# Optimization experiments

Measured on AMD Instinct MI355X. Metric: run time of the kernel, lower is better.

The kernel has to match this reference:

```python
import jax, jax.numpy as jnp
import numpy as np
import math

BS, SEQ, LQ = 64, 2048, 128
NHEADS, D_TIME, NH, DV = 4, 128, 128, 2
D_K = D_TIME // NHEADS
T10_LO, T10_HI = 0.1, 5.0
M0_LO, M0_HI = 0.1, 10.0
XFA_MAX_DEG = 25.0
REG_H = 200


def setup_inputs() -> dict:
    key = jax.random.key(0)
    ks = jax.random.split(key, 40)
    w = lambda i, shape, s=0.05: jax.random.normal(ks[i], shape, dtype=jnp.float32) * s
    return {
        "X_fa_in": jax.random.uniform(ks[0], (BS, SEQ), dtype=jnp.float32),
        "fa_vals": jax.random.uniform(ks[1], (BS, SEQ), dtype=jnp.float32),
        "fa_mask": jax.random.bernoulli(ks[2], 0.7, (BS, SEQ)),
        "fa_len": jnp.full((BS, 1), float(SEQ), dtype=jnp.float32),
        "TR_vals": jax.random.uniform(ks[3], (BS, SEQ), dtype=jnp.float32),
        "te_lin_w": w(4, (1, 1)), "te_lin_b": w(5, (1,)),
        "te_per_w": w(6, (D_TIME - 1, 1), 1.0), "te_per_b": w(7, (D_TIME - 1,)),
        "q_w": w(8, (D_TIME, D_TIME)), "q_b": w(9, (D_TIME,)),
        "k_w": w(10, (D_TIME, D_TIME)), "k_b": w(11, (D_TIME,)),
        "att_out_w": w(12, (NH, NHEADS * DV)), "att_out_b": w(13, (NH,)),
        "gru_wih": w(14, (3 * NH, NH)), "gru_whh": w(15, (3 * NH, NH)),
        "gru_bih": w(16, (3 * NH,)), "gru_bhh": w(17, (3 * NH,)),
        "score_t10_w": w(18, (1, NH)), "score_m0_w": w(19, (1, NH)),
        "regT_w1": w(20, (REG_H, NH)), "regT_b1": w(21, (REG_H,)),
        "regT_w2": w(22, (REG_H, REG_H)), "regT_b2": w(23, (REG_H,)),
        "regT_w3": w(24, (1, REG_H)), "regT_b3": w(25, (1,)),
        "regM_w1": w(26, (REG_H, NH)), "regM_b1": w(27, (REG_H,)),
        "regM_w2": w(28, (REG_H, REG_H)), "regM_b2": w(29, (REG_H,)),
        "regM_w3": w(30, (1, REG_H)), "regM_b3": w(31, (1,)),
    }


def _time_embed(t, lw, lb, pw, pb):
    # t: (..., L) -> (..., L, D_TIME); linear(1->1) concat sin(linear(1->D_TIME-1))
    t = t[..., None]
    lin = t * lw[0, 0] + lb                      # (..., L, 1)
    per = jnp.sin(t @ pw.T + pb)                 # (..., L, D_TIME-1)
    return jnp.concatenate([lin, per], axis=-1)


def _gru(x, wih, whh, bih, bhh):
    # x: (bs, T, NH) -> (bs, T, NH), torch nn.GRU semantics, h0 = 0
    x_gates = jnp.einsum('bth,gh->btg', x, wih) + bih  # (bs, T, 3*NH)

    def step(h, xt):
        gh = h @ whh.T + bhh
        ri, zi, ni = jnp.split(xt, 3, axis=-1)
        rh, zh, nh = jnp.split(gh, 3, axis=-1)
        r = jax.nn.sigmoid(ri + rh)
        z = jax.nn.sigmoid(zi + zh)
        n = jnp.tanh(ni + r * nh)
        hn = (1.0 - z) * n + z * h
        return hn, hn

    h0 = jnp.zeros((x.shape[0], whh.shape[1]), dtype=x.dtype)
    _, hs = jax.lax.scan(step, h0, x_gates.transpose(1, 0, 2))
    return hs.transpose(1, 0, 2)


def _mlp(h, w1, b1, w2, b2, w3, b3):
    h = jax.nn.gelu(h @ w1.T + b1, approximate=False)
    h = jax.nn.gelu(h @ w2.T + b2, approximate=False)
    return h @ w3.T + b3


def reference(X_fa_in, fa_vals, fa_mask, fa_len, TR_vals,
              te_lin_w, te_lin_b, te_per_w, te_per_b,
              q_w, q_b, k_w, k_b, att_out_w, att_out_b,
              gru_wih, gru_whh, gru_bih, gru_bhh,
              score_t10_w, score_m0_w,
              regT_w1, regT_b1, regT_w2, regT_b2, regT_w3, regT_b3,
              regM_w1, regM_b1, regM_w2, regM_b2, regM_w3, regM_b3):
    bs, seq = X_fa_in.shape
    # ---- time embeddings (dropout inactive / eval) ----
    key_input = fa_vals / math.radians(XFA_MAX_DEG - 1.0)
    k_emb = _time_embed(key_input, te_lin_w, te_lin_b, te_per_w, te_per_b)   # (bs, seq, D_TIME)
    q_ref = jnp.linspace(0.0, 1.0, LQ, dtype=X_fa_in.dtype)[None, :]         # (1, LQ)
    q_emb = _time_embed(q_ref, te_lin_w, te_lin_b, te_per_w, te_per_b)       # (1, LQ, D_TIME)

    # ---- multi-time attention ----
    q = (q_emb @ q_w.T + q_b).reshape(1, LQ, NHEADS, D_K).transpose(0, 2, 1, 3)[0]  # (h, LQ, d_k)
    k = (k_emb @ k_w.T + k_b).reshape(bs, seq, NHEADS, D_K).transpose(0, 2, 1, 3)    # (bs, h, seq, d_k)
    scores = jnp.einsum('hqd,bhsd->bhqs', q, k) / jnp.sqrt(jnp.asarray(D_K, X_fa_in.dtype))
    # mask is broadcast identically across the d_v replication in the original,
    # so the per-channel softmax collapses to one softmax over keys.
    scores = jnp.where(fa_mask[:, None, None, :], scores, jnp.asarray(-1e9, scores.dtype))
    p = jax.nn.softmax(scores, axis=-1)                                      # (bs, h, LQ, seq)
    v = jnp.concatenate([X_fa_in[..., None], fa_mask.astype(X_fa_in.dtype)[..., None]], axis=-1)  # (bs, seq, 2)
    attn = jnp.einsum('bhqs,bsd->bhqd', p, v)                                # (bs, h, LQ, 2)
    concat = attn.transpose(0, 2, 1, 3).reshape(bs, LQ, NHEADS * DV)
    att_out = concat @ att_out_w.T + att_out_b                               # (bs, LQ, NH)

    # ---- GRU + attention pooling ----
    out = _gru(att_out, gru_wih, gru_whh, gru_bih, gru_bhh)                  # (bs, LQ, NH)
    sT = jax.nn.softmax(out @ score_t10_w.T, axis=1)                         # (bs, LQ, 1)
    sM = jax.nn.softmax(out @ score_m0_w.T, axis=1)
    hidden_T10 = jnp.sum(out * sT, axis=1)                                   # (bs, NH)
    hidden_M0 = jnp.sum(out * sM, axis=1)

    T10 = T10_LO + jax.nn.sigmoid(_mlp(hidden_T10, regT_w1, regT_b1, regT_w2, regT_b2, regT_w3, regT_b3)) * (T10_HI - T10_LO)  # (bs, 1)
    M0 = M0_LO + jax.nn.sigmoid(_mlp(hidden_M0, regM_w1, regM_b1, regM_w2, regM_b2, regM_w3, regM_b3)) * (M0_HI - M0_LO)       # (bs, 1)
    R1 = 1.0 / T10
    E = jnp.exp(-TR_vals * R1)                                               # (bs, seq)
    X_out = (1.0 - E) * jnp.sin(fa_vals) / (1.0 - jnp.cos(fa_vals) * E) * M0
    return (X_out, T10, M0)
```

## Files before the change

### kernel.cpp

```cpp
#include <hip/hip_runtime.h>

#define BS 64
#define SEQ 2048
#define LQ 128
#define NH 128

typedef short bf16x8 __attribute__((ext_vector_type(8)));
typedef float f32x4 __attribute__((ext_vector_type(4)));
typedef unsigned short u16x4 __attribute__((ext_vector_type(4)));
typedef unsigned uint2v __attribute__((ext_vector_type(2)));

__device__ __forceinline__ unsigned short f2bf(float f) {
  unsigned u = __float_as_uint(f);
  u = (u + 0x7FFFu + ((u >> 16) & 1u)) >> 16;
  return (unsigned short)u;
}
__device__ __forceinline__ float b2f(unsigned short u) {
  return __uint_as_float((unsigned)u << 16);
}
__device__ __forceinline__ float sigm(float x) { return 1.f / (1.f + __expf(-x)); }
__device__ __forceinline__ float gelu_f(float x) { return 0.5f * x * (1.f + erff(x * 0.70710678118654752f)); }
__device__ __forceinline__ float fexp2(float x) { float y; asm("v_exp_f32 %0, %1" : "=v"(y) : "v"(x)); return y; }
__device__ __forceinline__ float frcp(float x) { float y; asm("v_rcp_f32 %0, %1" : "=v"(y) : "v"(x)); return y; }
__device__ __forceinline__ unsigned cvtpk(float lo, float hi) {
  unsigned d; asm("v_cvt_pk_bf16_f32 %0, %1, %2" : "=v"(d) : "v"(lo), "v"(hi)); return d;
}

__device__ __forceinline__ void softbar() {
  asm volatile("s_waitcnt lgkmcnt(0)" ::: "memory");
  __builtin_amdgcn_s_barrier();
  __builtin_amdgcn_sched_barrier(0);
}

__global__ __launch_bounds__(384) void k_prep(
    const void* __restrict__ mraw,
    const float* __restrict__ qw, const float* __restrict__ qb,
    const float* __restrict__ lw, const float* __restrict__ lb,
    const float* __restrict__ pw, const float* __restrict__ pb,
    const float* __restrict__ wih, const float* __restrict__ bih,
    const float* __restrict__ bhh,
    const float* __restrict__ aow, const float* __restrict__ aob,
    float* __restrict__ maskb, unsigned short* __restrict__ qbf,
    float* __restrict__ fwc) {
  const int tid = threadIdx.x;
  const int blk = blockIdx.x;
  if (blk < 342) {
    __shared__ int sflag;
    if (tid < 64) {
      const unsigned* raw = (const unsigned*)mraw;
      int isf = 0, isb = 0;
#pragma unroll
      for (int k = 0; k < 4; ++k) {
        unsigned w = raw[tid + k * 64];
        isf |= (w == 0x3F800000u);
        isb |= (w > 1u);
      }
      isf = __any(isf);
      isb = __any(isb);
      if (tid == 0) sflag = isf ? 2 : (isb ? 1 : 0);
    }
    __syncthreads();
    int fl = sflag;
    int i = blk * 384 + tid;
    if (i < BS * SEQ) {
      bool on;
      if (fl == 2)      on = (((const float*)mraw)[i] != 0.f);
      else if (fl == 1) on = (((const unsigned char*)mraw)[i] != 0);
      else              on = (((const int*)mraw)[i] != 0);
      maskb[i] = on ? 0.f : -30000.f;
    }
  } else if (blk < 350) {
    __shared__ float emb[16 * 132];
    __shared__ float Ac[128], Bc[128];
    const int sb = blk - 342;
    const float C2 = 0.25505654f;
    if (tid < 128) {
      Ac[tid] = (tid == 0) ? lw[0] : pw[tid - 1];
      Bc[tid] = (tid == 0) ? lb[0] : pb[tid - 1];
    }
    __syncthreads();
    if (tid < 256) {
      int lq = tid >> 4, e0 = (tid & 15) * 8;
      float tv = (float)(sb * 16 + lq) * (1.f / 127.f);
#pragma unroll
      for (int k = 0; k < 8; ++k) {
        int e = e0 + k;
        float arg = fmaf(tv, Ac[e], Bc[e]);
        emb[lq * 132 + e] = (e == 0) ? arg : __sinf(arg);
      }
    }
    __syncthreads();
    if (tid < 256) {
      const int c = tid & 127, lh = tid >> 7;
      float acc[8];
#pragma unroll
      for (int i = 0; i < 8; ++i) acc[i] = qb[c];
      for (int e4 = 0; e4 < 32; ++e4) {
        float4 wv = *(const float4*)(qw + c * 128 + e4 * 4);
#pragma unroll
        for (int i = 0; i < 8; ++i) {
          const float* er = &emb[(lh * 8 + i) * 132 + e4 * 4];
          acc[i] += wv.x * er[0] + wv.y * er[1] + wv.z * er[2] + wv.w * er[3];
        }
      }
#pragma unroll
      for (int i = 0; i < 8; ++i) {
        int lq = sb * 16 + lh * 8 + i;
        qbf[((c >> 5) * LQ + lq) * 32 + (c & 31)] = f2bf(acc[i] * C2);
      }
    }
  } else {
    const int g = tid;
    const float sc = (g < 256) ? -1.4426950408889634f : 2.8853900817779268f;
    float fw[8];
#pragma unroll
    for (int c = 0; c < 8; ++c) fw[c] = 0.f;
    float cg = bih[g] + (g < 256 ? bhh[g] : 0.f);
    for (int j = 0; j < 128; ++j) {
      float w = wih[g * 128 + j];
      cg = fmaf(w, aob[j], cg);
#pragma unroll
      for (int c = 0; c < 8; ++c) fw[c] = fmaf(w, aow[j * 8 + c], fw[c]);
    }
#pragma unroll
    for (int c = 0; c < 8; ++c) fwc[g * 12 + c] = fw[c] * sc;
    fwc[g * 12 + 8] = cg * sc;
  }
}

__global__ __launch_bounds__(384) void k_xgate(
    const float* __restrict__ fwc, const float* __restrict__ part,
    unsigned short* __restrict__ xg) {
  __shared__ float at[64][8];
  const int tid = threadIdx.x;
  const int t = blockIdx.x;
  if (tid < 256) {
    int b = tid >> 2, h = tid & 3;
    const float* p = part + ((size_t)(b * LQ + t) * 4 + h) * 8;
    float4 p0 = *(const float4*)p;
    float4 p1 = *(const float4*)(p + 4);
    float a = p0.x + p0.z + p1.x + p1.z;
    float l = p0.y + p0.w + p1.y + p1.w;
    at[b][h * 2] = a / l;
    at[b][h * 2 + 1] = 1.f;
  }
  __syncthreads();
  const int q = tid >> 2, s = tid & 3;
  float wv[4][8], cg[4];
#pragma unroll
  for (int j = 0; j < 4; ++j) {
    int row = q * 4 + j;
    float4 a0 = *(const float4*)(fwc + row * 12);
    float4 a1 = *(const float4*)(fwc + row * 12 + 4);
    wv[j][0] = a0.x; wv[j][1] = a0.y; wv[j][2] = a0.z; wv[j][3] = a0.w;
    wv[j][4] = a1.x; wv[j][5] = a1.y; wv[j][6] = a1.z; wv[j][7] = a1.w;
    cg[j] = fwc[row * 12 + 8];
  }
  unsigned short* obase = xg + (((size_t)t * 96 + q) * 64 + s * 16) * 4;
#pragma unroll 4
  for (int bb = 0; bb < 16; ++bb) {
    const float* a = at[s * 16 + bb];
    u16x4 o;
#pragma unroll
    for (int j = 0; j < 4; ++j) {
      float acc = cg[j] + wv[j][0] * a[0] + wv[j][1] * a[1] + wv[j][2] * a[2] + wv[j][3] * a[3]
                        + wv[j][4] * a[4] + wv[j][5] * a[5] + wv[j][6] * a[6] + wv[j][7] * a[7];
      o[j] = f2bf(acc);
    }
    *(u16x4*)(obase + bb * 4) = o;
  }
}

__global__ __launch_bounds__(256) void k_attn(
    const float* __restrict__ Xfa, const float* __restrict__ maskb,
    const float* __restrict__ fav,
    const float* __restrict__ kw, const float* __restrict__ kb,
    const float* __restrict__ lw, const float* __restrict__ lb,
    const float* __restrict__ pw, const float* __restrict__ pb,
    const unsigned short* __restrict__ qbf,
    float* __restrict__ part) {
  __shared__ unsigned short kwl[128 * 136];
  __shared__ unsigned short ktl[2][64 * 136];
  __shared__ float xt[2][64], mtl[2][64], kbl[128], Ac[128], Bc[128];

  const int tid = threadIdx.x;
  const int lane = tid & 63, wave = tid >> 6;
  const int l15 = lane & 15, kg = lane >> 4;
  const int b = blockIdx.x >> 2, qt = blockIdx.x & 3;
  const float KSCALE = 2.3873241463784303f;

  if (tid < 128) {
    Ac[tid] = (tid == 0) ? lw[0] : pw[tid - 1];
    Bc[tid] = (tid == 0) ? lb[0] : pb[tid - 1];
    kbl[tid] = kb[tid];
  }
  for (int idx = tid; idx < 2048; idx += 256) {
    int d = idx >> 4, e0 = (idx & 15) * 8;
    const float* src = kw + d * 128 + e0;
    float4 s0 = *(const float4*)(src);
    float4 s1 = *(const float4*)(src + 4);
    bf16x8 v;
    v[0] = (short)f2bf(s0.x); v[1] = (short)f2bf(s0.y);
    v[2] = (short)f2bf(s0.z); v[3] = (short)f2bf(s0.w);
    v[4] = (short)f2bf(s1.x); v[5] = (short)f2bf(s1.y);
    v[6] = (short)f2bf(s1.z); v[7] = (short)f2bf(s1.w);
    *(bf16x8*)&kwl[d * 136 + e0] = v;
  }
  bf16x8 qa[4][2];
#pragma unroll
  for (int h = 0; h < 4; ++h)
#pragma unroll
    for (int mt = 0; mt < 2; ++mt) {
      int qrow = (wave * 2 + mt) * 16 + l15;
      qa[h][mt] = *(const bf16x8*)(qbf + (h * 128 + qrow) * 32 + kg * 8);
    }
  float sl[4][2][4], sa[4][2][4];
#pragma unroll
  for (int h = 0; h < 4; ++h)
#pragma unroll
    for (int mt = 0; mt < 2; ++mt)
#pragma unroll
      for (int r = 0; r < 4; ++r) { sl[h][mt][r] = 0.f; sa[h][mt][r] = 0.f; }
  __syncthreads();

#define ATTN_STAGE(TT)                                                                   \
  {                                                                                      \
    const int tt_ = (TT);                                                                \
    const int ss0 = qt * 512 + tt_ * 64;                                                 \
    float tv = fav[b * SEQ + ss0 + wave * 16 + l15] * KSCALE;                            \
    float xfv = 0.f, mbv = 0.f;                                                          \
    if (tid < 64) {                                                                      \
      xfv = Xfa[b * SEQ + ss0 + tid];                                                    \
      mbv = maskb[b * SEQ + ss0 + tid];                                                  \
    }                                                                                    \
    bf16x8 af[4];                                                                        \
    _Pragma("unroll")                                                                    \
    for (int kp = 0; kp < 4; ++kp) {                                                     \
      bf16x8 v;                                                                          \
      _Pragma("unroll")                                                                  \
      for (int j = 0; j < 8; ++j) {                                                      \
        int e = kp * 32 + kg * 8 + j;                                                    \
        float arg = fmaf(tv, Ac[e], Bc[e]);                                              \
        float val = (e == 0) ? arg : __sinf(arg);                                        \
        v[j] = (short)f2bf(val);                                                         \
      }                                                                                  \
      af[kp] = v;                                                                        \
    }                                                                                    \
    _Pragma("unroll")                                                                    \
    for (int h = 0; h < 4; ++h) {                                                        \
      _Pragma("unroll")                                                                  \
      for (int nt = 0; nt < 2; ++nt) {                                                   \
        f32x4 acc = {0.f, 0.f, 0.f, 0.f};                                                \
        _Pragma("unroll")                                                                \
        for (int kp = 0; kp < 4; ++kp) {                                                 \
          bf16x8 bb = *(const bf16x8*)&kwl[(h * 32 + nt * 16 + l15) * 136 + kp * 32 + kg * 8]; \
          acc = __builtin_amdgcn_mfma_f32_16x16x32_bf16(af[kp], bb, acc, 0, 0, 0);       \
        }                                                                                \
        int d = nt * 16 + l15;                                                           \
        float kbv = kbl[h * 32 + d];                                                     \
        _Pragma("unroll")                                                                \
        for (int r = 0; r < 4; ++r) {                                                    \
          int srow = wave * 16 + kg * 4 + r;                                             \
          ktl[tt_ & 1][srow * 136 + h * 32 + d] = f2bf(acc[r] + kbv);                    \
        }                                                                                \
      }                                                                                  \
    }                                                                                    \
    if (tid < 64) {                                                                      \
      xt[tt_ & 1][tid] = xfv;                                                            \
      mtl[tt_ & 1][tid] = mbv;                                                           \
    }                                                                                    \
  }

  ATTN_STAGE(0);
  softbar();
#pragma unroll 1
  for (int t8 = 0; t8 < 8; ++t8) {
    const int cur = t8 & 1;
    {
      float xv[4], mv[4];
#pragma unroll
      for (int nt2 = 0; nt2 < 4; ++nt2) {
        int scol = nt2 * 16 + l15;
        xv[nt2] = xt[cur][scol];
        mv[nt2] = mtl[cur][scol];
      }
#pragma unroll
      for (int h = 0; h < 4; ++h) {
        f32x4 D[2][4];
#pragma unroll
        for (int nt2 = 0; nt2 < 4; ++nt2) {
          int scol = nt2 * 16 + l15;
          bf16x8 bk = *(const bf16x8*)&ktl[cur][scol * 136 + h * 32 + kg * 8];
#pragma unroll
          for (int mt = 0; mt < 2; ++mt) {
            f32x4 z = {0.f, 0.f, 0.f, 0.f};
            D[mt][nt2] = __builtin_amdgcn_mfma_f32_16x16x32_bf16(qa[h][mt], bk, z, 0, 0, 0);
          }
        }
#pragma unroll
        for (int mt = 0; mt < 2; ++mt)
#pragma unroll
          for (int r = 0; r < 4; ++r) {
            float p0 = fexp2(D[mt][0][r] + mv[0]);
            float p1 = fexp2(D[mt][1][r] + mv[1]);
            float p2 = fexp2(D[mt][2][r] + mv[2]);
            float p3 = fexp2(D[mt][3][r] + mv[3]);
            sl[h][mt][r] += (p0 + p1) + (p2 + p3);
            sa[h][mt][r] += fmaf(p0, xv[0], fmaf(p1, xv[1], fmaf(p2, xv[2], p3 * xv[3])));
          }
      }
    }
    if (t8 < 7) ATTN_STAGE(t8 + 1);
    softbar();
  }
#undef ATTN_STAGE
#pragma unroll
  for (int h = 0; h < 4; ++h)
#pragma unroll
    for (int mt = 0; mt < 2; ++mt)
#pragma unroll
      for (int r = 0; r < 4; ++r) {
        float l = sl[h][mt][r], a = sa[h][mt][r];
#pragma unroll
        for (int off = 1; off <= 8; off <<= 1) {
          l += __shfl_xor(l, off);
          a += __shfl_xor(a, off);
        }
        if (l15 == 0) {
          int q = (wave * 2 + mt) * 16 + kg * 4 + r;
          float* p = part + ((size_t)(b * LQ + q) * 4 + h) * 8 + qt * 2;
          p[0] = a;
          p[1] = l;
        }
      }
}

__global__ __launch_bounds__(512) void k_gru9(
    const float* __restrict__ whh, const float* __restrict__ bhh,
    const unsigned short* __restrict__ xg, unsigned short* __restrict__ gout) {
  __shared__ unsigned short hbf[2][16][132];
  const int tid = threadIdx.x;
  const int lane = tid & 63, w = tid >> 6;
  const int l15 = lane & 15, kg = lane >> 4;
  const int b0 = blockIdx.x * 16;

  for (int i = tid; i < 2 * 16 * 132 / 2; i += 512) ((unsigned*)hbf)[i] = 0u;

  bf16x8 wfr[3][4];
#pragma unroll
  for (int n = 0; n < 3; ++n) {
    const float sc = (n < 2) ? -1.4426950408889634f : 2.8853900817779268f;
    const float* wrow = whh + (n * 128 + w * 16 + l15) * 128 + kg * 8;
#pragma unroll
    for (int kk = 0; kk < 4; ++kk) {
      float4 f0 = *(const float4*)(wrow + kk * 32);
      float4 f1 = *(const float4*)(wrow + kk * 32 + 4);
      bf16x8 v;
      v[0] = (short)f2bf(f0.x * sc); v[1] = (short)f2bf(f0.y * sc);
      v[2] = (short)f2bf(f0.z * sc); v[3] = (short)f2bf(f0.w * sc);
      v[4] = (short)f2bf(f1.x * sc); v[5] = (short)f2bf(f1.y * sc);
      v[6] = (short)f2bf(f1.z * sc); v[7] = (short)f2bf(f1.w * sc);
      wfr[n][kk] = v;
    }
  }
  f32x4 bhnv;
  {
    float4 t = *(const float4*)(bhh + 256 + w * 16 + kg * 4);
    bhnv[0] = t.x * 2.8853900817779268f; bhnv[1] = t.y * 2.8853900817779268f;
    bhnv[2] = t.z * 2.8853900817779268f; bhnv[3] = t.w * 2.8853900817779268f;
  }
  float hold[4] = {0.f, 0.f, 0.f, 0.f};

  const unsigned short* xlane = xg + (((size_t)(w * 4 + kg)) * 64 + b0 + l15) * 4;
  unsigned short* gptr = gout + (size_t)(b0 + l15) * LQ * NH + w * 16 + kg * 4;

  u16x4 xA[2][3], xB[2][3];
#pragma unroll
  for (int s = 0; s < 2; ++s)
#pragma unroll
    for (int n = 0; n < 3; ++n)
      xA[s][n] = *(const u16x4*)(xlane + (size_t)s * 24576 + n * 8192);
  __syncthreads();

#define GRU_STEP(T, XQ)                                                                 \
  {                                                                                     \
    const int t_ = (T);                                                                 \
    bf16x8 hf[4];                                                                       \
    _Pragma("unroll")                                                                   \
    for (int kk = 0; kk < 4; ++kk)                                                      \
      hf[kk] = *(const bf16x8*)&hbf[t_ & 1][l15][kg * 8 + kk * 32];                     \
    f32x4 c0, c1;                                                                       \
    _Pragma("unroll")                                                                   \
    for (int r = 0; r < 4; ++r) { c0[r] = b2f(XQ[0][r]); c1[r] = b2f(XQ[1][r]); }       \
    f32x4 z4 = {0.f, 0.f, 0.f, 0.f};                                                    \
    f32x4 p0 = __builtin_amdgcn_mfma_f32_16x16x32_bf16(wfr[0][0], hf[0], c0, 0, 0, 0);  \
    p0 = __builtin_amdgcn_mfma_f32_16x16x32_bf16(wfr[0][1], hf[1], p0, 0, 0, 0);        \
    f32x4 q0 = __builtin_amdgcn_mfma_f32_16x16x32_bf16(wfr[0][2], hf[2], z4, 0, 0, 0);  \
    q0 = __builtin_amdgcn_mfma_f32_16x16x32_bf16(wfr[0][3], hf[3], q0, 0, 0, 0);        \
    f32x4 p1 = __builtin_amdgcn_mfma_f32_16x16x32_bf16(wfr[1][0], hf[0], c1, 0, 0, 0);  \
    p1 = __builtin_amdgcn_mfma_f32_16x16x32_bf16(wfr[1][1], hf[1], p1, 0, 0, 0);        \
    f32x4 q1 = __builtin_amdgcn_mfma_f32_16x16x32_bf16(wfr[1][2], hf[2], z4, 0, 0, 0);  \
    q1 = __builtin_amdgcn_mfma_f32_16x16x32_bf16(wfr[1][3], hf[3], q1, 0, 0, 0);        \
    f32x4 p2 = __builtin_amdgcn_mfma_f32_16x16x32_bf16(wfr[2][0], hf[0], bhnv, 0, 0, 0);\
    p2 = __builtin_amdgcn_mfma_f32_16x16x32_bf16(wfr[2][1], hf[1], p2, 0, 0, 0);        \
    f32x4 q2 = __builtin_amdgcn_mfma_f32_16x16x32_bf16(wfr[2][2], hf[2], z4, 0, 0, 0);  \
    q2 = __builtin_amdgcn_mfma_f32_16x16x32_bf16(wfr[2][3], hf[3], q2, 0, 0, 0);        \
    f32x4 a0 = p0 + q0, a1 = p1 + q1, a2 = p2 + q2;                                     \
    float hv[4];                                                                        \
    _Pragma("unroll")                                                                   \
    for (int r = 0; r < 4; ++r) {                                                       \
      float R = frcp(1.f + fexp2(a0[r]));                                               \
      float Z = frcp(1.f + fexp2(a1[r]));                                               \
      float u = fmaf(R, a2[r], b2f(XQ[2][r]));                                          \
      float Tt = frcp(1.f + fexp2(u));                                                  \
      float ng = fmaf(-2.f, Tt, 1.f);                                                   \
      float hn = fmaf(Z, hold[r] - ng, ng);                                             \
      hold[r] = hn;                                                                     \
      hv[r] = hn;                                                                       \
    }                                                                                   \
    uint2v d;                                                                           \
    d[0] = cvtpk(hv[0], hv[1]);                                                         \
    d[1] = cvtpk(hv[2], hv[3]);                                                         \
    *(uint2v*)&hbf[(t_ & 1) ^ 1][l15][w * 16 + kg * 4] = d;                             \
    *(uint2v*)(gptr + (size_t)t_ * NH) = d;                                             \
    softbar();                                                                          \
  }

#define GRU_PAIR(TP, XC, XN)                                                            \
  {                                                                                     \
    const int tp_ = (TP);                                                               \
    const int tl = (tp_ < 63) ? (tp_ + 1) : 63;                                         \
    _Pragma("unroll")                                                                   \
    for (int s = 0; s < 2; ++s)                                                         \
      _Pragma("unroll")                                                                 \
      for (int n = 0; n < 3; ++n)                                                       \
        XN[s][n] = *(const u16x4*)(xlane + ((size_t)(tl * 2 + s)) * 24576 + n * 8192);  \
    GRU_STEP(tp_ * 2, XC[0]);                                                           \
    GRU_STEP(tp_ * 2 + 1, XC[1]);                                                       \
  }

#pragma unroll 1
  for (int tp = 0; tp < 64; tp += 2) {
    GRU_PAIR(tp, xA, xB);
    GRU_PAIR(tp + 1, xB, xA);
  }
#undef GRU_PAIR
#undef GRU_STEP
}

__global__ __launch_bounds__(256) void k_heads(
    const unsigned short* __restrict__ gout,
    const float* __restrict__ swT, const float* __restrict__ swM,
    const float* __restrict__ tw1, const float* __restrict__ tb1,
    const float* __restrict__ tw2, const float* __restrict__ tb2,
    const float* __restrict__ tw3, const float* __restrict__ tb3,
    const float* __restrict__ mw1, const float* __restrict__ mb1,
    const float* __restrict__ mw2, const float* __restrict__ mb2,
    const float* __restrict__ mw3, const float* __restrict__ mb3,
    const float* __restrict__ fav, const float* __restrict__ TRv,
    float* __restrict__ out) {
  __shared__ float hbuf[128 * 129];
  __shared__ float pp[2][128][2];
  __shared__ float pT[128], pM[128];
  __shared__ float hidT[128], hidM[128];
  __shared__ float l1b[200], l2b[200];
  __shared__ float parts[4];
  __shared__ float scal[2];
  const int tid = threadIdx.x;
  const int b = blockIdx.x;
#pragma unroll
  for (int rep = 0; rep < 8; ++rep) {
    int idx = rep * 2048 + tid * 8;
    int row = idx >> 7, col = idx & 127;
    bf16x8 v = *(const bf16x8*)(gout + (size_t)b * (LQ * NH) + idx);
#pragma unroll
    for (int j = 0; j < 8; ++j)
      hbuf[row * 129 + col + j] = b2f((unsigned short)v[j]);
  }
  __syncthreads();
  {
    int t = tid & 127, hf2 = tid >> 7;
    float aT = 0.f, aM = 0.f;
    for (int j = 0; j < 64; ++j) {
      float v = hbuf[t * 129 + hf2 * 64 + j];
      aT = fmaf(v, swT[hf2 * 64 + j], aT);
      aM = fmaf(v, swM[hf2 * 64 + j], aM);
    }
    pp[hf2][t][0] = aT;
    pp[hf2][t][1] = aM;
  }
  __syncthreads();
  if (tid < 64) {
    float v0 = pp[0][tid][0] + pp[1][tid][0];
    float v1 = pp[0][tid + 64][0] + pp[1][tid + 64][0];
    float m = fmaxf(v0, v1);
    for (int off = 32; off > 0; off >>= 1) m = fmaxf(m, __shfl_xor(m, off));
    float p0 = __expf(v0 - m), p1 = __expf(v1 - m);
    float s = p0 + p1;
    for (int off = 32; off > 0; off >>= 1) s += __shfl_xor(s, off);
    float inv = 1.f / s;
    pT[tid] = p0 * inv; pT[tid + 64] = p1 * inv;
  } else if (tid < 128) {
    int l = tid - 64;
    float v0 = pp[0][l][1] + pp[1][l][1];
    float v1 = pp[0][l + 64][1] + pp[1][l + 64][1];
    float m = fmaxf(v0, v1);
    for (int off = 32; off > 0; off >>= 1) m = fmaxf(m, __shfl_xor(m, off));
    float p0 = __expf(v0 - m), p1 = __expf(v1 - m);
    float s = p0 + p1;
    for (int off = 32; off > 0; off >>= 1) s += __shfl_xor(s, off);
    float inv = 1.f / s;
    pM[l] = p0 * inv; pM[l + 64] = p1 * inv;
  }
  __syncthreads();
  {
    int j = tid & 127, hf2 = tid >> 7;
    float aT = 0.f, aM = 0.f;
    for (int t2 = 0; t2 < 64; ++t2) {
      int t = hf2 * 64 + t2;
      float v = hbuf[t * 129 + j];
      aT = fmaf(v, pT[t], aT);
      aM = fmaf(v, pM[t], aM);
    }
    pp[hf2][j][0] = aT;
    pp[hf2][j][1] = aM;
  }
  __syncthreads();
  if (tid < 128) {
    hidT[tid] = pp[0][tid][0] + pp[1][tid][0];
    hidM[tid] = pp[0][tid][1] + pp[1][tid][1];
  }
  __syncthreads();
#pragma unroll 1
  for (int hd = 0; hd < 2; ++hd) {
    const float* in = hd ? hidM : hidT;
    const float* w1 = hd ? mw1 : tw1; const float* b1 = hd ? mb1 : tb1;
    const float* w2 = hd ? mw2 : tw2; const float* b2 = hd ? mb2 : tb2;
    const float* w3 = hd ? mw3 : tw3; const float* b3 = hd ? mb3 : tb3;
    if (tid < 200) {
      float acc = b1[tid];
      for (int j4 = 0; j4 < 32; ++j4) {
        float4 wv = *(const float4*)(w1 + tid * 128 + j4 * 4);
        acc += wv.x * in[j4 * 4] + wv.y * in[j4 * 4 + 1] + wv.z * in[j4 * 4 + 2] + wv.w * in[j4 * 4 + 3];
      }
      l1b[tid] = gelu_f(acc);
    }
    __syncthreads();
    if (tid < 200) {
      float acc = b2[tid];
      for (int k4 = 0; k4 < 50; ++k4) {
        float4 wv = *(const float4*)(w2 + tid * 200 + k4 * 4);
        acc += wv.x * l1b[k4 * 4] + wv.y * l1b[k4 * 4 + 1] + wv.z * l1b[k4 * 4 + 2] + wv.w * l1b[k4 * 4 + 3];
      }
      l2b[tid] = gelu_f(acc);
    }
    __syncthreads();
    float part = (tid < 200) ? l2b[tid] * w3[tid] : 0.f;
    for (int off = 32; off > 0; off >>= 1) part += __shfl_xor(part, off);
    if ((tid & 63) == 0) parts[tid >> 6] = part;
    __syncthreads();
    if (tid == 0) {
      float y = parts[0] + parts[1] + parts[2] + parts[3] + b3[0];
      float hi = hd ? 10.f : 5.f;
      float val = 0.1f + sigm(y) * (hi - 0.1f);
      scal[hd] = val;
      out[BS * SEQ + hd * BS + b] = val;
    }
    __syncthreads();
  }
  float T10 = scal[0], M0 = scal[1];
  float R1 = 1.f / T10;
  for (int i = tid; i < SEQ; i += 256) {
    float fa = fav[b * SEQ + i];
    float tr = TRv[b * SEQ + i];
    float E = __expf(-tr * R1);
    float s, c;
    __sincosf(fa, &s, &c);
    out[b * SEQ + i] = (1.f - E) * s / (1.f - c * E) * M0;
  }
}

extern "C" void kernel_launch(void* const* d_in, const int* in_sizes, int n_in,
                              void* d_out, int out_size, void* d_ws, size_t ws_size,
                              hipStream_t stream) {
  const float* Xfa = (const float*)d_in[0];
  const float* fav = (const float*)d_in[1];
  const void*  mraw = d_in[2];
  const float* TRv = (const float*)d_in[4];
  const float* lw = (const float*)d_in[5];
  const float* lb = (const float*)d_in[6];
  const float* pw = (const float*)d_in[7];
  const float* pb = (const float*)d_in[8];
  const float* qw = (const float*)d_in[9];
  const float* qb = (const float*)d_in[10];
  const float* kw = (const float*)d_in[11];
  const float* kb = (const float*)d_in[12];
  const float* aow = (const float*)d_in[13];
  const float* aob = (const float*)d_in[14];
  const float* wih = (const float*)d_in[15];
  const float* whh = (const float*)d_in[16];
  const float* bih = (const float*)d_in[17];
  const float* bhh = (const float*)d_in[18];
  const float* swT = (const float*)d_in[19];
  const float* swM = (const float*)d_in[20];
  const float* tw1 = (const float*)d_in[21];
  const float* tb1 = (const float*)d_in[22];
  const float* tw2 = (const float*)d_in[23];
  const float* tb2 = (const float*)d_in[24];
  const float* tw3 = (const float*)d_in[25];
  const float* tb3 = (const float*)d_in[26];
  const float* mw1 = (const float*)d_in[27];
  const float* mb1 = (const float*)d_in[28];
  const float* mw2 = (const float*)d_in[29];
  const float* mb2 = (const float*)d_in[30];
  const float* mw3 = (const float*)d_in[31];
  const float* mb3 = (const float*)d_in[32];
  float* out = (float*)d_out;
  char* ws = (char*)d_ws;

  unsigned short* qbf = (unsigned short*)ws;
  float* part = (float*)(ws + 32768);
  unsigned short* gout = (unsigned short*)(ws + 32768);
  float* fwc = (float*)(ws + 2129920);
  float* maskb = (float*)(ws + 2148352);
  unsigned short* xgate = (unsigned short*)(ws + 2672768);

  k_prep<<<351, 384, 0, stream>>>(mraw, qw, qb, lw, lb, pw, pb,
                                  wih, bih, bhh, aow, aob, maskb, qbf, fwc);
  k_attn<<<256, 256, 0, stream>>>(Xfa, maskb, fav, kw, kb, lw, lb, pw, pb, qbf, part);
  k_xgate<<<128, 384, 0, stream>>>(fwc, part, xgate);
  k_gru9<<<4, 512, 0, stream>>>(whh, bhh, xgate, gout);
  k_heads<<<64, 256, 0, stream>>>(gout, swT, swM, tw1, tb1, tw2, tb2, tw3, tb3,
                                  mw1, mb1, mw2, mb2, mw3, mb3, fav, TRv, out);
}
```

Before: 178.6 us.

## Fuse mask decoding into attention kernel and batch GRU output stores

Mask-type detection and mask-to-bias conversion move from a separate pass in k_prep into k_attn, which now reads the raw mask directly. This removes the 512KB maskb workspace round trip and shrinks k_prep from 351 blocks to 9. Separately, the GRU kernel buffers four timesteps of hidden output in registers and writes them together, instead of issuing a global store every step inside the serial recurrence. The cost is some extra branching in the attention load path and a few more live registers in the GRU.

```diff
diff --git a/kernel.cpp b/kernel.cpp
--- a/kernel.cpp
+++ b/kernel.cpp
@@ -33,46 +33,18 @@
 }
 
 __global__ __launch_bounds__(384) void k_prep(
-    const void* __restrict__ mraw,
     const float* __restrict__ qw, const float* __restrict__ qb,
     const float* __restrict__ lw, const float* __restrict__ lb,
     const float* __restrict__ pw, const float* __restrict__ pb,
     const float* __restrict__ wih, const float* __restrict__ bih,
     const float* __restrict__ bhh,
     const float* __restrict__ aow, const float* __restrict__ aob,
-    float* __restrict__ maskb, unsigned short* __restrict__ qbf,
-    float* __restrict__ fwc) {
+    unsigned short* __restrict__ qbf, float* __restrict__ fwc) {
   const int tid = threadIdx.x;
   const int blk = blockIdx.x;
-  if (blk < 342) {
-    __shared__ int sflag;
-    if (tid < 64) {
-      const unsigned* raw = (const unsigned*)mraw;
-      int isf = 0, isb = 0;
-#pragma unroll
-      for (int k = 0; k < 4; ++k) {
-        unsigned w = raw[tid + k * 64];
-        isf |= (w == 0x3F800000u);
-        isb |= (w > 1u);
-      }
-      isf = __any(isf);
-      isb = __any(isb);
-      if (tid == 0) sflag = isf ? 2 : (isb ? 1 : 0);
-    }
-    __syncthreads();
-    int fl = sflag;
-    int i = blk * 384 + tid;
-    if (i < BS * SEQ) {
-      bool on;
-      if (fl == 2)      on = (((const float*)mraw)[i] != 0.f);
-      else if (fl == 1) on = (((const unsigned char*)mraw)[i] != 0);
-      else              on = (((const int*)mraw)[i] != 0);
-      maskb[i] = on ? 0.f : -30000.f;
-    }
-  } else if (blk < 350) {
+  if (blk < 8) {
     __shared__ float emb[16 * 132];
     __shared__ float Ac[128], Bc[128];
-    const int sb = blk - 342;
     const float C2 = 0.25505654f;
     if (tid < 128) {
       Ac[tid] = (tid == 0) ? lw[0] : pw[tid - 1];
@@ -81,7 +53,7 @@
     __syncthreads();
     if (tid < 256) {
       int lq = tid >> 4, e0 = (tid & 15) * 8;
-      float tv = (float)(sb * 16 + lq) * (1.f / 127.f);
+      float tv = (float)(blk * 16 + lq) * (1.f / 127.f);
 #pragma unroll
       for (int k = 0; k < 8; ++k) {
         int e = e0 + k;
@@ -105,7 +77,7 @@
       }
 #pragma unroll
       for (int i = 0; i < 8; ++i) {
-        int lq = sb * 16 + lh * 8 + i;
+        int lq = blk * 16 + lh * 8 + i;
         qbf[((c >> 5) * LQ + lq) * 32 + (c & 31)] = f2bf(acc[i] * C2);
       }
     }
@@ -172,7 +144,7 @@
 }
 
 __global__ __launch_bounds__(256) void k_attn(
-    const float* __restrict__ Xfa, const float* __restrict__ maskb,
+    const float* __restrict__ Xfa, const void* __restrict__ mraw,
     const float* __restrict__ fav,
     const float* __restrict__ kw, const float* __restrict__ kb,
     const float* __restrict__ lw, const float* __restrict__ lb,
@@ -182,6 +154,7 @@
   __shared__ unsigned short kwl[128 * 136];
   __shared__ unsigned short ktl[2][64 * 136];
   __shared__ float xt[2][64], mtl[2][64], kbl[128], Ac[128], Bc[128];
+  __shared__ int sflag;
 
   const int tid = threadIdx.x;
   const int lane = tid & 63, wave = tid >> 6;
@@ -193,6 +166,19 @@
     Ac[tid] = (tid == 0) ? lw[0] : pw[tid - 1];
     Bc[tid] = (tid == 0) ? lb[0] : pb[tid - 1];
     kbl[tid] = kb[tid];
+  }
+  if (wave == 3) {
+    const unsigned* raw = (const unsigned*)mraw;
+    int isf = 0, isb = 0;
+#pragma unroll
+    for (int k = 0; k < 4; ++k) {
+      unsigned w2 = raw[lane + k * 64];
+      isf |= (w2 == 0x3F800000u);
+      isb |= (w2 > 1u);
+    }
+    isf = __any(isf);
+    isb = __any(isb);
+    if (lane == 0) sflag = isf ? 2 : (isb ? 1 : 0);
   }
   for (int idx = tid; idx < 2048; idx += 256) {
     int d = idx >> 4, e0 = (idx & 15) * 8;
@@ -222,6 +208,7 @@
 #pragma unroll
       for (int r = 0; r < 4; ++r) { sl[h][mt][r] = 0.f; sa[h][mt][r] = 0.f; }
   __syncthreads();
+  const int mfl = sflag;
 
 #define ATTN_STAGE(TT)                                                                   \
   {                                                                                      \
@@ -230,8 +217,13 @@
     float tv = fav[b * SEQ + ss0 + wave * 16 + l15] * KSCALE;                            \
     float xfv = 0.f, mbv = 0.f;                                                          \
     if (tid < 64) {                                                                      \
-      xfv = Xfa[b * SEQ + ss0 + tid];                                                    \
-      mbv = maskb[b * SEQ + ss0 + tid];                                                  \
+      int gi = b * SEQ + ss0 + tid;                                                      \
+      xfv = Xfa[gi];                                                                     \
+      bool on;                                                                           \
+      if (mfl == 2)      on = (((const float*)mraw)[gi] != 0.f);                         \
+      else if (mfl == 1) on = (((const unsigned char*)mraw)[gi] != 0);                   \
+      else               on = (((const int*)mraw)[gi] != 0);                             \
+      mbv = on ? 0.f : -30000.f;                                                         \
     }                                                                                    \
     bf16x8 af[4];                                                                        \
     _Pragma("unroll")                                                                    \
@@ -335,7 +327,7 @@
       }
 }
 
-__global__ __launch_bounds__(512) void k_gru9(
+__global__ __launch_bounds__(512) void k_gru10(
     const float* __restrict__ whh, const float* __restrict__ bhh,
     const unsigned short* __restrict__ xg, unsigned short* __restrict__ gout) {
   __shared__ unsigned short hbf[2][16][132];
@@ -375,6 +367,7 @@
   unsigned short* gptr = gout + (size_t)(b0 + l15) * LQ * NH + w * 16 + kg * 4;
 
   u16x4 xA[2][3], xB[2][3];
+  uint2v gb0, gb1, gb2, gb3;
 #pragma unroll
   for (int s = 0; s < 2; ++s)
 #pragma unroll
@@ -382,7 +375,7 @@
       xA[s][n] = *(const u16x4*)(xlane + (size_t)s * 24576 + n * 8192);
   __syncthreads();
 
-#define GRU_STEP(T, XQ)                                                                 \
+#define GRU_STEP(T, XQ, PH)                                                             \
   {                                                                                     \
     const int t_ = (T);                                                                 \
     bf16x8 hf[4];                                                                       \
@@ -422,11 +415,21 @@
     d[0] = cvtpk(hv[0], hv[1]);                                                         \
     d[1] = cvtpk(hv[2], hv[3]);                                                         \
     *(uint2v*)&hbf[(t_ & 1) ^ 1][l15][w * 16 + kg * 4] = d;                             \
-    *(uint2v*)(gptr + (size_t)t_ * NH) = d;                                             \
+    if ((PH) == 0) gb0 = d;                                                             \
+    if ((PH) == 1) gb1 = d;                                                             \
+    if ((PH) == 2) gb2 = d;                                                             \
+    if ((PH) == 3) {                                                                    \
+      gb3 = d;                                                                          \
+      unsigned short* gp = gptr + (size_t)(t_ - 3) * NH;                                \
+      *(uint2v*)(gp) = gb0;                                                             \
+      *(uint2v*)(gp + NH) = gb1;                                                        \
+      *(uint2v*)(gp + 2 * NH) = gb2;                                                    \
+      *(uint2v*)(gp + 3 * NH) = gb3;                                                    \
+    }                                                                                   \
     softbar();                                                                          \
   }
 
-#define GRU_PAIR(TP, XC, XN)                                                            \
+#define GRU_PAIR(TP, XC, XN, PH0, PH1)                                                  \
   {                                                                                     \
     const int tp_ = (TP);                                                               \
     const int tl = (tp_ < 63) ? (tp_ + 1) : 63;                                         \
@@ -435,14 +438,14 @@
       _Pragma("unroll")                                                                 \
       for (int n = 0; n < 3; ++n)                                                       \
         XN[s][n] = *(const u16x4*)(xlane + ((size_t)(tl * 2 + s)) * 24576 + n * 8192);  \
-    GRU_STEP(tp_ * 2, XC[0]);                                                           \
-    GRU_STEP(tp_ * 2 + 1, XC[1]);                                                       \
+    GRU_STEP(tp_ * 2, XC[0], PH0);                                                      \
+    GRU_STEP(tp_ * 2 + 1, XC[1], PH1);                                                  \
   }
 
 #pragma unroll 1
   for (int tp = 0; tp < 64; tp += 2) {
-    GRU_PAIR(tp, xA, xB);
-    GRU_PAIR(tp + 1, xB, xA);
+    GRU_PAIR(tp, xA, xB, 0, 1);
+    GRU_PAIR(tp + 1, xB, xA, 2, 3);
   }
 #undef GRU_PAIR
 #undef GRU_STEP
@@ -622,14 +625,13 @@
   float* part = (float*)(ws + 32768);
   unsigned short* gout = (unsigned short*)(ws + 32768);
   float* fwc = (float*)(ws + 2129920);
-  float* maskb = (float*)(ws + 2148352);
-  unsigned short* xgate = (unsigned short*)(ws + 2672768);
-
-  k_prep<<<351, 384, 0, stream>>>(mraw, qw, qb, lw, lb, pw, pb,
-                                  wih, bih, bhh, aow, aob, maskb, qbf, fwc);
-  k_attn<<<256, 256, 0, stream>>>(Xfa, maskb, fav, kw, kb, lw, lb, pw, pb, qbf, part);
+  unsigned short* xgate = (unsigned short*)(ws + 2148352);
+
+  k_prep<<<9, 384, 0, stream>>>(qw, qb, lw, lb, pw, pb,
+                                wih, bih, bhh, aow, aob, qbf, fwc);
+  k_attn<<<256, 256, 0, stream>>>(Xfa, mraw, fav, kw, kb, lw, lb, pw, pb, qbf, part);
   k_xgate<<<128, 384, 0, stream>>>(fwc, part, xgate);
-  k_gru9<<<4, 512, 0, stream>>>(whh, bhh, xgate, gout);
+  k_gru10<<<4, 512, 0, stream>>>(whh, bhh, xgate, gout);
   k_heads<<<64, 256, 0, stream>>>(gout, swT, swM, tw1, tb1, tw2, tb2, tw3, tb3,
                                   mw1, mb1, mw2, mb2, mw3, mb3, fav, TRv, out);
 }
```

Measured after the change: 209.9 us. +17.5%, slower.
